# Performance work log

Hardware: AMD Instinct MI355X
Metric: run time of the kernel (lower is better)

Reference implementation:

```python
import jax, jax.numpy as jnp
import numpy as np

NUM_NEURONS = 8192
BATCH = 2048
TAU = 20.0
DT = 1.0
AR_WEIGHT = 0.5


def setup_inputs() -> dict:
    key = jax.random.key(0)
    k1, k2 = jax.random.split(key)
    input_current = jax.random.normal(k1, (BATCH, NUM_NEURONS), dtype=jnp.float32)
    u = jax.random.uniform(k2, (BATCH, NUM_NEURONS), dtype=jnp.float32)
    v0 = jnp.zeros((NUM_NEURONS,), dtype=jnp.float32)  # initial membrane potential
    return {"input_current": input_current, "u": u, "v0": v0}


def _row_spikes(v, u_row):
    """Autoregressive Bernoulli sampling across neurons for one batch row.
    p_i = sigmoid(V_i + w * spike_{i-1}); spike_i = 1[u_i < p_i]."""
    def neuron_step(prev_spike, xs):
        vj, uj = xs
        p = jax.nn.sigmoid(vj + AR_WEIGHT * prev_spike)
        s = (uj < p).astype(jnp.float32)
        return s, s
    _, spikes = jax.lax.scan(neuron_step, jnp.float32(0.0), (v, u_row))
    return spikes


def reference(input_current, u, v0):
    alpha = DT / TAU
    def batch_step(v, xs):
        i_row, u_row = xs
        # LIF membrane update (vectorized over neurons); state persists across rows
        v = v + alpha * (-v + i_row)
        spikes = _row_spikes(v, u_row)
        return v, spikes
    _, out = jax.lax.scan(batch_step, v0, (input_current, u))
    return out  # (BATCH, NUM_NEURONS) float32 binary spikes
```

## Files before the change

kernel.cpp:

```cpp
#include <hip/hip_runtime.h>

#define NEURONS 8192
#define BATCH_N 2048
#define GROUP 32
#define CHUNK_ROWS 512
#define WARMUP 512

__device__ __forceinline__ float ref_sigmoid(float zf) {
    double z = -(double)zf;
    const double LOG2E  = 1.4426950408889634074;
    const double LN2_HI = 6.93147180369123816490e-01;
    const double LN2_LO = 1.90821492927058770002e-10;
    double kd = __builtin_rint(z * LOG2E);
    double r  = __builtin_fma(-kd, LN2_HI, z);
    r         = __builtin_fma(-kd, LN2_LO, r);
    double p;
    p = 2.7557319223985888e-07;
    p = __builtin_fma(p, r, 2.7557319223985893e-06);
    p = __builtin_fma(p, r, 2.4801587301587302e-05);
    p = __builtin_fma(p, r, 1.9841269841269841e-04);
    p = __builtin_fma(p, r, 1.3888888888888889e-03);
    p = __builtin_fma(p, r, 8.3333333333333332e-03);
    p = __builtin_fma(p, r, 4.1666666666666664e-02);
    p = __builtin_fma(p, r, 1.6666666666666666e-01);
    p = __builtin_fma(p, r, 5.0e-01);
    p = __builtin_fma(p, r, 1.0);
    p = __builtin_fma(p, r, 1.0);
    long long ki = (long long)kd;
    double two_k = __longlong_as_double((unsigned long long)(ki + 1023) << 52);
    float ef = (float)(p * two_k);
    return __fdiv_rn(1.0f, __fadd_rn(1.0f, ef));
}

template <bool STORE>
__device__ __forceinline__ float lif_span(const float* __restrict__ ip,
                                          float* __restrict__ vp, float v) {
    const float alpha = 0.05f;
    float buf0[GROUP], buf1[GROUP];
    #pragma unroll
    for (int k = 0; k < GROUP; ++k) buf0[k] = ip[(size_t)k * NEURONS];

    const int NGROUPS = CHUNK_ROWS / GROUP;
    for (int g = 0; g < NGROUPS; g += 2) {
        {
            const float* p = ip + (size_t)(g + 1) * GROUP * NEURONS;
            #pragma unroll
            for (int k = 0; k < GROUP; ++k) buf1[k] = p[(size_t)k * NEURONS];
        }
        {
            float* q = vp + (size_t)g * GROUP * NEURONS;
            #pragma unroll
            for (int k = 0; k < GROUP; ++k) {
                v = __fadd_rn(v, __fmul_rn(alpha, __fadd_rn(buf0[k], -v)));
                if constexpr (STORE) q[(size_t)k * NEURONS] = v;
            }
        }
        if (g + 2 < NGROUPS) {
            const float* p = ip + (size_t)(g + 2) * GROUP * NEURONS;
            #pragma unroll
            for (int k = 0; k < GROUP; ++k) buf0[k] = p[(size_t)k * NEURONS];
        }
        {
            float* q = vp + (size_t)(g + 1) * GROUP * NEURONS;
            #pragma unroll
            for (int k = 0; k < GROUP; ++k) {
                v = __fadd_rn(v, __fmul_rn(alpha, __fadd_rn(buf1[k], -v)));
                if constexpr (STORE) q[(size_t)k * NEURONS] = v;
            }
        }
    }
    return v;
}

__global__ __launch_bounds__(64) void lif_v_kernel(const float* __restrict__ I,
                                                   const float* __restrict__ V0,
                                                   float* __restrict__ V) {
    int nb    = blockIdx.x & 127;
    int chunk = blockIdx.x >> 7;
    int j = nb * 64 + (int)threadIdx.x;
    float v = V0[j];
    int row0 = chunk * CHUNK_ROWS;
    if (chunk > 0) {
        const float* ip = I + (size_t)(row0 - WARMUP) * NEURONS + j;
        v = lif_span<false>(ip, nullptr, v);
    }
    const float* ip = I + (size_t)row0 * NEURONS + j;
    float*       vp = V + (size_t)row0 * NEURONS + j;
    lif_span<true>(ip, vp, v);
}

__global__ __launch_bounds__(256) void spike_kernel(const float* __restrict__ U,
                                                    float* __restrict__ VS) {
    int gtid = blockIdx.x * 256 + threadIdx.x;
    int wave = gtid >> 6;
    int lane = gtid & 63;
    const size_t row = (size_t)wave * NEURONS;
    const float* u_row = U + row;
    float* vs_row = VS + row;
    const unsigned long long ltmask =
        (lane == 0) ? 0ull : (~0ull >> (64 - lane));

    float4 cv = *reinterpret_cast<const float4*>(vs_row + lane * 4);
    float4 cu = *reinterpret_cast<const float4*>(u_row + lane * 4);

    int carry = 0;
    for (int c = 0; c < NEURONS; c += 256) {
        int base = c + lane * 4;
        int nbase = (c + 256 < NEURONS) ? (base + 256) : base;
        float4 nv = *reinterpret_cast<const float4*>(vs_row + nbase);
        float4 nu = *reinterpret_cast<const float4*>(u_row + nbase);

        float vv[4] = {cv.x, cv.y, cv.z, cv.w};
        float uu[4] = {cu.x, cu.y, cu.z, cu.w};

        int s0[4], s1[4];
        #pragma unroll
        for (int k = 0; k < 4; ++k) {
            float p0 = ref_sigmoid(vv[k]);
            float p1 = ref_sigmoid(__fadd_rn(vv[k], 0.5f));
            s0[k] = (uu[k] < p0) ? 1 : 0;
            s1[k] = (uu[k] < p1) ? 1 : 0;
        }

        int st0 = 0, st1 = 1;
        #pragma unroll
        for (int k = 0; k < 4; ++k) {
            st0 = st0 ? s1[k] : s0[k];
            st1 = st1 ? s1[k] : s0[k];
        }

        unsigned long long constMask = __ballot(st0 == st1);
        unsigned long long valMask   = __ballot(st0 != 0);
        unsigned long long below = constMask & ltmask;
        int cin = below ? (int)((valMask >> (63 - __clzll(below))) & 1ull)
                        : carry;

        int s = cin;
        float out[4];
        #pragma unroll
        for (int k = 0; k < 4; ++k) {
            s = s ? s1[k] : s0[k];
            out[k] = (float)s;
        }
        *reinterpret_cast<float4*>(vs_row + base) =
            make_float4(out[0], out[1], out[2], out[3]);

        carry = __shfl(s, 63);
        cv = nv; cu = nu;
    }
}

extern "C" void kernel_launch(void* const* d_in, const int* in_sizes, int n_in,
                              void* d_out, int out_size, void* d_ws, size_t ws_size,
                              hipStream_t stream) {
    const float* I  = (const float*)d_in[0];
    const float* U  = (const float*)d_in[1];
    const float* V0 = (const float*)d_in[2];
    float* OUT = (float*)d_out;

    (void)in_sizes; (void)n_in; (void)out_size; (void)d_ws; (void)ws_size;

    lif_v_kernel<<<512, 64, 0, stream>>>(I, V0, OUT);
    spike_kernel<<<(BATCH_N * 64) / 256, 256, 0, stream>>>(U, OUT);
}
```

Before: 214.1 us.

## Split each spike row across four waves with two-hypothesis carry composition

The spike kernel now assigns one block per batch row and splits each row into four 2048-neuron segments, one per wave. Each wave evaluates its segment under both possible incoming carries and packs the spike bits into registers. The waves then combine segment carries through shared memory and write out the matching result. This raises parallelism from one wave per row to four, which shortens the serial 32-chunk chain per row. In exchange it doubles the scan-path work, holds outputs in registers until the end, and adds a block barrier.

```diff
diff --git a/kernel.cpp b/kernel.cpp
--- a/kernel.cpp
+++ b/kernel.cpp
@@ -5,6 +5,7 @@
 #define GROUP 32
 #define CHUNK_ROWS 512
 #define WARMUP 512
+#define SEG 2048
 
 __device__ __forceinline__ float ref_sigmoid(float zf) {
     double z = -(double)zf;
@@ -91,24 +92,27 @@
 
 __global__ __launch_bounds__(256) void spike_kernel(const float* __restrict__ U,
                                                     float* __restrict__ VS) {
-    int gtid = blockIdx.x * 256 + threadIdx.x;
-    int wave = gtid >> 6;
-    int lane = gtid & 63;
-    const size_t row = (size_t)wave * NEURONS;
-    const float* u_row = U + row;
-    float* vs_row = VS + row;
+    __shared__ int m0s[4], m1s[4];
+    int row  = blockIdx.x;
+    int wid  = threadIdx.x >> 6;
+    int lane = threadIdx.x & 63;
+    const size_t rbase = (size_t)row * NEURONS;
+    const float* u_seg = U  + rbase + wid * SEG;
+    float*      vs_seg = VS + rbase + wid * SEG;
     const unsigned long long ltmask =
         (lane == 0) ? 0ull : (~0ull >> (64 - lane));
 
-    float4 cv = *reinterpret_cast<const float4*>(vs_row + lane * 4);
-    float4 cu = *reinterpret_cast<const float4*>(u_row + lane * 4);
+    float4 cv = *reinterpret_cast<const float4*>(vs_seg + lane * 4);
+    float4 cu = *reinterpret_cast<const float4*>(u_seg + lane * 4);
 
-    int carry = 0;
-    for (int c = 0; c < NEURONS; c += 256) {
-        int base = c + lane * 4;
-        int nbase = (c + 256 < NEURONS) ? (base + 256) : base;
-        float4 nv = *reinterpret_cast<const float4*>(vs_row + nbase);
-        float4 nu = *reinterpret_cast<const float4*>(u_row + nbase);
+    unsigned int out_a = 0, out_b = 0;
+    int a = 0, b = 1;
+    #pragma unroll
+    for (int c8 = 0; c8 < 8; ++c8) {
+        int base  = c8 * 256 + lane * 4;
+        int nbase = (c8 < 7) ? (base + 256) : base;
+        float4 nv = *reinterpret_cast<const float4*>(vs_seg + nbase);
+        float4 nu = *reinterpret_cast<const float4*>(u_seg + nbase);
 
         float vv[4] = {cv.x, cv.y, cv.z, cv.w};
         float uu[4] = {cu.x, cu.y, cu.z, cu.w};
@@ -131,22 +135,41 @@
 
         unsigned long long constMask = __ballot(st0 == st1);
         unsigned long long valMask   = __ballot(st0 != 0);
-        unsigned long long below = constMask & ltmask;
-        int cin = below ? (int)((valMask >> (63 - __clzll(below))) & 1ull)
-                        : carry;
+        unsigned long long below     = constMask & ltmask;
+        int vb  = below ? (int)((valMask >> (63 - __clzll(below))) & 1ull) : 0;
+        int has = below ? 1 : 0;
+        int cin0 = has ? vb : 0;
+        int cin1 = has ? vb : 1;
 
-        int s = cin;
-        float out[4];
+        int sA = cin0, sB = cin1;
+        unsigned int o0 = 0, o1 = 0;
         #pragma unroll
         for (int k = 0; k < 4; ++k) {
-            s = s ? s1[k] : s0[k];
-            out[k] = (float)s;
+            sA = sA ? s1[k] : s0[k];  o0 |= (unsigned)sA << k;
+            sB = sB ? s1[k] : s0[k];  o1 |= (unsigned)sB << k;
         }
-        *reinterpret_cast<float4*>(vs_row + base) =
-            make_float4(out[0], out[1], out[2], out[3]);
+        int t0 = __shfl(sA, 63);
+        int t1 = __shfl(sB, 63);
 
-        carry = __shfl(s, 63);
+        out_a |= (a ? o1 : o0) << (4 * c8);
+        out_b |= (b ? o1 : o0) << (4 * c8);
+        a = a ? t1 : t0;
+        b = b ? t1 : t0;
         cv = nv; cu = nu;
+    }
+
+    if (lane == 0) { m0s[wid] = a; m1s[wid] = b; }
+    __syncthreads();
+    int cin = 0;
+    for (int i = 0; i < wid; ++i) cin = cin ? m1s[i] : m0s[i];
+    unsigned int bits = cin ? out_b : out_a;
+
+    #pragma unroll
+    for (int c8 = 0; c8 < 8; ++c8) {
+        unsigned int nib = bits >> (4 * c8);
+        *reinterpret_cast<float4*>(vs_seg + c8 * 256 + lane * 4) =
+            make_float4((float)(nib & 1), (float)((nib >> 1) & 1),
+                        (float)((nib >> 2) & 1), (float)((nib >> 3) & 1));
     }
 }
 
@@ -161,5 +184,5 @@
     (void)in_sizes; (void)n_in; (void)out_size; (void)d_ws; (void)ws_size;
 
     lif_v_kernel<<<512, 64, 0, stream>>>(I, V0, OUT);
-    spike_kernel<<<(BATCH_N * 64) / 256, 256, 0, stream>>>(U, OUT);
+    spike_kernel<<<BATCH_N, 256, 0, stream>>>(U, OUT);
 }
```

New measurement: 212.4 us. No clear change (-0.8%).
